# Kernel tuning notes

Hardware: AMD Instinct MI355X
Metric: run time of the kernel (lower is better)

The kernel has to match this reference:

```python
import jax, jax.numpy as jnp
import numpy as np

EPS = 1e-8


def l2norm(x, axis):
    # matches torch: x / (sqrt(sum(x^2)) + eps)
    return x / (jnp.sqrt(jnp.sum(x * x, axis=axis, keepdims=True)) + EPS)


def setup_inputs() -> dict:
    key = jax.random.key(0)
    k1, k2, k3, k4, k5 = jax.random.split(key, 5)
    I, C, L, R, D = 16, 32, 32, 36, 1024  # n_image, n_caption, max_words, n_regions, embed_dim
    img_emb = l2norm(jax.random.normal(k1, (I, R, D), jnp.float32), -1)
    cap_emb = l2norm(jax.random.normal(k2, (C, L, D), jnp.float32), -1)
    W_emb = jax.random.normal(k3, (D, D), jnp.float32)  # nn.Embedding weight, N(0,1) default init
    sim_map_w = 2.5 + 0.1 * jax.random.normal(k4, (1, D), jnp.float32)  # init_weight: normal(2.5, 0.1)
    temp_scale_w = jnp.full((1, 1), np.log(1.0 / 0.07), jnp.float32)    # init_weight
    temp_learnable_w = jnp.full((1, 1), 4.0, jnp.float32)               # init_weight
    cap_lens = jax.random.randint(k5, (C,), 4, L + 1, jnp.int32)        # ragged caption lengths in [4, L]
    return dict(img_emb=img_emb, cap_emb=cap_emb, W_emb=W_emb, sim_map_w=sim_map_w,
                temp_scale_w=temp_scale_w, temp_learnable_w=temp_learnable_w, cap_lens=cap_lens)


def reference(img_emb, cap_emb, W_emb, sim_map_w, temp_scale_w, temp_learnable_w, cap_lens):
    D = W_emb.shape[0]
    L = cap_emb.shape[1]
    # --- dimension-weight branch (caption-independent) ---
    # linspace(0, D, D).long(): last index is D (out of range in torch); gather with clip.
    idx = jnp.floor(jnp.linspace(0.0, D, D)).astype(jnp.int32)
    weights = jax.nn.sigmoid(jnp.take(W_emb, idx, axis=0, mode='clip'))  # (D, D)
    mean_p = jnp.mean(weights, axis=1)                  # (D,)
    std_p = jnp.std(weights, axis=1, ddof=1)            # torch.std is unbiased
    thres = mean_p + sim_map_w[0] * std_p               # (D,)
    values = jnp.exp(temp_learnable_w[0, 0]) * (weights - thres[:, None])
    mask_p = jnp.tanh(jnp.exp(values))
    Dlw = l2norm(mask_p * weights, axis=1)              # Dim_learned_weights (D, D)
    diag = Dlw.sum(0)                                   # Diagonal (D,); diag_embed matmul == elementwise scale
    smooth = jnp.exp(temp_scale_w[0, 0])
    # --- vectorized ragged per-caption cross attention ---
    wmask = (jnp.arange(L)[None, :] < cap_lens[:, None]).astype(cap_emb.dtype)  # (C, L)
    # attn[c,i,l,r] = tanh(sum_d cap[c,l,d] * diag[d] * img[i,r,d])
    attn = jnp.tanh(jnp.einsum('cld,ird->cilr', cap_emb, img_emb * diag))
    attn = jnp.where(attn >= 0, attn, 0.1 * attn) * wmask[:, None, :, None]  # LeakyReLU(0.1), zero padded words
    attn = attn / (jnp.sqrt(jnp.sum(attn * attn, axis=2, keepdims=True)) + EPS)  # l2norm over word dim
    attn = jax.nn.softmax(attn * smooth, axis=3)        # softmax over regions
    ctx = l2norm(jnp.einsum('cilr,ird->cild', attn, img_emb), axis=-1)  # Context_img
    sim_loc = ctx * cap_emb[:, None, :, :]
    sim_sub = jnp.einsum('cild,ed->cile', sim_loc, Dlw)  # sim_loc @ Dlw.T
    sim_vec = l2norm(sim_sub, axis=-1).sum(-1)           # (C, I, L)
    # mean over the n_word valid words of each caption
    sim = jnp.sum(sim_vec * wmask[:, None, :], axis=2) / cap_lens[:, None].astype(cap_emb.dtype)  # (C, I)
    return sim.T  # (n_image, n_caption), matching torch.cat(sim_all, 1)
```

## Files before the change

### kernel.cpp

```cpp
#include <hip/hip_runtime.h>
#include <hip/hip_bf16.h>

#define I_N 16
#define C_N 32
#define L_N 32
#define R_N 36
#define D_N 1024
#define EPSF 1e-8f

typedef _Float16 f16;
typedef __attribute__((ext_vector_type(8))) _Float16 half8;
typedef __attribute__((ext_vector_type(4))) float floatx4;

__device__ __forceinline__ void gl16(const f16* g, f16* l) {
  __builtin_amdgcn_global_load_lds(
      (const __attribute__((address_space(1))) void*)g,
      (__attribute__((address_space(3))) void*)l, 16, 0, 0);
}

__device__ __forceinline__ float fast_tanh(float x) {
  float q = __expf(-2.f * fabsf(x));
  float t = (1.f - q) / (1.f + q);
  return (x >= 0.f) ? t : -t;
}

__device__ __forceinline__ float blk_sum_256(float v, float* red) {
  #pragma unroll
  for (int off = 32; off > 0; off >>= 1) v += __shfl_down(v, off, 64);
  int wid = threadIdx.x >> 6;
  if ((threadIdx.x & 63) == 0) red[wid] = v;
  __syncthreads();
  float s = red[0] + red[1] + red[2] + red[3];
  __syncthreads();
  return s;
}

__global__ __launch_bounds__(256) void k_dlw(const float* __restrict__ W,
    const float* __restrict__ simw, const float* __restrict__ tlw,
    const float* __restrict__ img,
    float* __restrict__ Dlw, f16* __restrict__ DlwH, f16* __restrict__ imgP) {
  int bid = blockIdx.x, tid = threadIdx.x;
  if (bid >= 1024) {
    int row = bid - 1024;
    int i = row / 48, r = row % 48;
    size_t dst = (size_t)row * D_N;
    if (r < R_N) {
      size_t src = ((size_t)i * R_N + r) * D_N;
      #pragma unroll
      for (int k = 0; k < 4; ++k) {
        int j = tid + k * 256;
        imgP[dst + j] = (f16)img[src + j];
      }
    } else {
      #pragma unroll
      for (int k = 0; k < 4; ++k) {
        int j = tid + k * 256;
        imgP[dst + j] = (f16)0.f;
      }
    }
    return;
  }
  int row = bid;
  __shared__ float red[4];
  const float* Wr = W + (size_t)row * D_N;
  float w[4]; float p = 0.f;
  #pragma unroll
  for (int k = 0; k < 4; ++k) {
    int j = tid + k * 256;
    float x = Wr[j];
    w[k] = 1.f / (1.f + __expf(-x));
    p += w[k];
  }
  float S = blk_sum_256(p, red);
  float mean = S * (1.f / 1024.f);
  p = 0.f;
  #pragma unroll
  for (int k = 0; k < 4; ++k) { float d = w[k] - mean; p += d * d; }
  float S2 = blk_sum_256(p, red);
  float stdv = sqrtf(S2 * (1.f / 1023.f));
  float thres = mean + simw[row] * stdv;
  float eT = __expf(tlw[0]);
  float mw[4]; p = 0.f;
  #pragma unroll
  for (int k = 0; k < 4; ++k) {
    float val = eT * (w[k] - thres);
    float y = __expf(val);
    float q = __expf(-2.f * y);
    float mp = (1.f - q) / (1.f + q);
    mw[k] = mp * w[k];
    p += mw[k] * mw[k];
  }
  float S3 = blk_sum_256(p, red);
  float inv = 1.f / (sqrtf(S3) + EPSF);
  #pragma unroll
  for (int k = 0; k < 4; ++k) {
    int j = tid + k * 256;
    float v = mw[k] * inv;
    Dlw[(size_t)row * D_N + j] = v;
    DlwH[(size_t)row * D_N + j] = (f16)v;
  }
}

__global__ __launch_bounds__(256) void k_dpp(const float* __restrict__ Dlw,
    const int* __restrict__ lens, float* __restrict__ dpart,
    int* __restrict__ pfx, int* __restrict__ mp) {
  int bid = blockIdx.x;
  if (bid < 64) {
    int p = bid >> 2;
    int col = (bid & 3) * 256 + threadIdx.x;
    float s = 0.f;
    #pragma unroll 8
    for (int r = p * 64; r < p * 64 + 64; ++r) s += Dlw[(size_t)r * D_N + col];
    dpart[(size_t)p * D_N + col] = s;
  } else if (threadIdx.x < 64) {
    int l = threadIdx.x;
    int v = (l < 32) ? lens[l] : 0;
    int s = v;
    #pragma unroll
    for (int off = 1; off < 32; off <<= 1) {
      int t = __shfl_up(s, off, 64);
      if (l >= off) s += t;
    }
    if (l < 32) pfx[l] = s - v;
    if (l == 31) { pfx[32] = s; mp[0] = s * 16; }
  }
}

__global__ __launch_bounds__(256) void k_capd(const float* __restrict__ dpart,
    const float* __restrict__ cap, f16* __restrict__ capD) {
  __shared__ float dg[D_N];
  int tid = threadIdx.x;
  #pragma unroll
  for (int k = 0; k < 4; ++k) {
    int col = tid + k * 256;
    float s = 0.f;
    #pragma unroll
    for (int p = 0; p < 16; ++p) s += dpart[(size_t)p * D_N + col];
    dg[col] = s;
  }
  __syncthreads();
  size_t base = (size_t)blockIdx.x * D_N;
  #pragma unroll
  for (int k = 0; k < 4; ++k) {
    int j = tid + k * 256;
    capD[base + j] = (f16)(cap[base + j] * dg[j]);
  }
}

__global__ __launch_bounds__(256) void k_qk(const f16* __restrict__ A,
    const f16* __restrict__ B, const int* __restrict__ lens,
    const float* __restrict__ tsw, float* __restrict__ pw) {
  int mt = blockIdx.x;
  int i  = blockIdx.y;
  int tid = threadIdx.x;
  int w = tid >> 6, lane = tid & 63;
  int l15 = lane & 15, h = lane >> 4;
  __shared__ __align__(16) f16 Als[64 * 32];
  __shared__ __align__(16) f16 Bls[48 * 32];
  __shared__ float att[64][49];
  __shared__ float cn[2][R_N];
  floatx4 acc[3];
  #pragma unroll
  for (int nf = 0; nf < 3; ++nf) acc[nf] = (floatx4)0.f;
  int arow = tid >> 2;
  int u = tid & 3;
  int vf = (u | ((arow & 1) << 2)) ^ ((arow >> 1) & 7);
  int wofs = (((arow & 62) | (vf >> 2)) * 32) + (vf & 3) * 8;
  const f16* Ag = A + (size_t)(mt * 64 + arow) * D_N + u * 8;
  const f16* Bg = B + (size_t)(i * 48 + arow) * D_N + u * 8;
  int v2 = (h | ((l15 & 1) << 2)) ^ ((l15 >> 1) & 7);
  int rbit = (v2 >> 2) & 1;
  int pun = (v2 & 3) * 8;
  int aoff = (w * 16 + (l15 & 14) + rbit) * 32 + pun;
  int boff[3];
  #pragma unroll
  for (int nf = 0; nf < 3; ++nf) boff[nf] = (nf * 16 + (l15 & 14) + rbit) * 32 + pun;
  for (int kk = 0; kk < D_N; kk += 32) {
    *(float4*)(&Als[wofs]) = *(const float4*)(Ag + kk);
    if (tid < 192) *(float4*)(&Bls[wofs]) = *(const float4*)(Bg + kk);
    __syncthreads();
    half8 a = *(const half8*)(&Als[aoff]);
    #pragma unroll
    for (int nf = 0; nf < 3; ++nf) {
      half8 b = *(const half8*)(&Bls[boff[nf]]);
      acc[nf] = __builtin_amdgcn_mfma_f32_16x16x32_f16(a, b, acc[nf], 0, 0, 0);
    }
    __syncthreads();
  }
  int len0 = lens[mt * 2], len1 = lens[mt * 2 + 1];
  #pragma unroll
  for (int nf = 0; nf < 3; ++nf)
    #pragma unroll
    for (int j = 0; j < 4; ++j) {
      int ml = w * 16 + h * 4 + j;
      int n = nf * 16 + l15;
      float t = fast_tanh(acc[nf][j]);
      float v = (t >= 0.f) ? t : 0.1f * t;
      int len = (ml >= 32) ? len1 : len0;
      if ((ml & 31) >= len || n >= R_N) v = 0.f;
      att[ml][n] = v;
    }
  __syncthreads();
  for (int e = tid; e < 2 * R_N; e += 256) {
    int cc = e / R_N, r = e % R_N;
    float s = 0.f;
    #pragma unroll
    for (int l = 0; l < 32; ++l) { float a = att[cc * 32 + l][r]; s += a * a; }
    cn[cc][r] = sqrtf(s) + EPSF;
  }
  __syncthreads();
  if (tid < 64) {
    int cc = tid >> 5, l = tid & 31;
    float smooth = __expf(tsw[0]);
    float mx = -3.4e38f;
    #pragma unroll
    for (int r = 0; r < R_N; ++r) {
      float z = att[tid][r] / cn[cc][r] * smooth;
      att[tid][r] = z;
      mx = fmaxf(mx, z);
    }
    float se = 0.f;
    #pragma unroll
    for (int r = 0; r < R_N; ++r) {
      float e2 = __expf(att[tid][r] - mx);
      att[tid][r] = e2;
      se += e2;
    }
    float inv = 1.f / se;
    float* dst = pw + ((size_t)i * 1024 + (mt * 2 + cc) * 32 + l) * R_N;
    #pragma unroll
    for (int r = 0; r < R_N; ++r) dst[r] = att[tid][r] * inv;
  }
}

__global__ __launch_bounds__(256) void k_ctx(const float* __restrict__ pw,
    const f16* __restrict__ imgP, const float* __restrict__ cap,
    const int* __restrict__ lens, const int* __restrict__ pfx,
    f16* __restrict__ slc) {
  int c  = blockIdx.x;
  int i  = blockIdx.y;
  int tid = threadIdx.x;
  int w = tid >> 6;
  int cg = tid & 63;
  int len = lens[c];
  int pf = pfx[c];
  __shared__ float pA[32][R_N];
  __shared__ __align__(16) f16 rows[R_N][1024];
  for (int e = tid; e < 32 * R_N; e += 256) {
    int rr = e / R_N, r = e % R_N;
    pA[rr][r] = pw[((size_t)i * 1024 + c * 32 + rr) * R_N + r];
  }
  const f16* base = imgP + (size_t)i * 48 * D_N;
  #pragma unroll
  for (int t = 0; t < 9; ++t) {
    int rr = w * 9 + t;
    const f16* src = base + (size_t)rr * D_N + cg * 8;
    gl16(src,       &rows[rr][0]);
    gl16(src + 512, &rows[rr][512]);
  }
  __syncthreads();
  int d0 = cg * 8, d1 = 512 + cg * 8;
  #pragma unroll
  for (int sub = 0; sub < 2; ++sub) {
    float acc[4][16];
    #pragma unroll
    for (int j = 0; j < 4; ++j)
      #pragma unroll
      for (int q = 0; q < 16; ++q) acc[j][q] = 0.f;
    for (int k = 0; k < R_N; ++k) {
      half8 h0 = *(const half8*)(&rows[k][d0]);
      half8 h1 = *(const half8*)(&rows[k][d1]);
      float bv[16];
      #pragma unroll
      for (int q = 0; q < 8; ++q) { bv[q] = (float)h0[q]; bv[8 + q] = (float)h1[q]; }
      #pragma unroll
      for (int j = 0; j < 4; ++j) {
        float a = pA[sub * 16 + w * 4 + j][k];
        #pragma unroll
        for (int q = 0; q < 16; ++q) acc[j][q] += a * bv[q];
      }
    }
    #pragma unroll
    for (int j = 0; j < 4; ++j) {
      int l = sub * 16 + w * 4 + j;
      float ss = 0.f;
      #pragma unroll
      for (int q = 0; q < 16; ++q) ss += acc[j][q] * acc[j][q];
      #pragma unroll
      for (int off = 1; off < 64; off <<= 1) ss += __shfl_xor(ss, off, 64);
      if (l < len) {
        float inv = 1.f / (sqrtf(ss) + EPSF);
        const float* capr = cap + ((size_t)c * L_N + l) * D_N;
        float4 c0 = *(const float4*)(capr + d0);
        float4 c1 = *(const float4*)(capr + d0 + 4);
        float4 c2 = *(const float4*)(capr + d1);
        float4 c3 = *(const float4*)(capr + d1 + 4);
        float cv[16] = {c0.x,c0.y,c0.z,c0.w, c1.x,c1.y,c1.z,c1.w,
                        c2.x,c2.y,c2.z,c2.w, c3.x,c3.y,c3.z,c3.w};
        union { f16 h[16]; float4 f4[2]; } u;
        #pragma unroll
        for (int q = 0; q < 16; ++q) u.h[q] = (f16)(acc[j][q] * inv * cv[q]);
        f16* dst = slc + ((size_t)((pf + l) * 16 + i)) * D_N;
        *(float4*)(dst + d0) = u.f4[0];
        *(float4*)(dst + d1) = u.f4[1];
      }
    }
  }
}

__global__ __launch_bounds__(256) void k_gemm(const f16* __restrict__ A,
    const f16* __restrict__ B, const int* __restrict__ mp,
    float* __restrict__ rs16, float* __restrict__ rq16) {
  int bx = blockIdx.x, by = blockIdx.y;
  int Mp = mp[0];
  int m0 = bx * 128, n0 = by * 128;
  if (m0 >= Mp) return;
  int tid = threadIdx.x;
  int w = tid >> 6, lane = tid & 63;
  int l15 = lane & 15, h = lane >> 4;
  int wm = w >> 1, wn = w & 1;
  __shared__ __align__(16) f16 AB[3][2][128 * 32];
  floatx4 acc[4][4];
  #pragma unroll
  for (int mf = 0; mf < 4; ++mf)
    #pragma unroll
    for (int nf = 0; nf < 4; ++nf) acc[mf][nf] = (floatx4)0.f;

  int r_p = lane >> 2, u_p = lane & 3;
  int sw = (r_p >> 1) & 7;
  int val = (u_p | ((r_p & 1) << 2)) ^ sw;
  int r_l = (r_p & 14) | (val >> 2);
  int u_l = val & 3;
  const f16* As0 = A + (size_t)(m0 + w * 32 +  0 + r_l) * D_N + u_l * 8;
  const f16* As1 = A + (size_t)(m0 + w * 32 + 16 + r_l) * D_N + u_l * 8;
  const f16* Bs0 = B + (size_t)(n0 + w * 32 +  0 + r_l) * D_N + u_l * 8;
  const f16* Bs1 = B + (size_t)(n0 + w * 32 + 16 + r_l) * D_N + u_l * 8;

  int v2 = (h | ((l15 & 1) << 2)) ^ ((l15 >> 1) & 7);
  int rbit = (v2 >> 2) & 1;
  int pun = (v2 & 3) * 8;
  int aoff[4], boff[4];
  #pragma unroll
  for (int f = 0; f < 4; ++f) {
    aoff[f] = (wm * 64 + f * 16 + (l15 & 14) + rbit) * 32 + pun;
    boff[f] = (wn * 64 + f * 16 + (l15 & 14) + rbit) * 32 + pun;
  }

  #define STAGE(kt, b) { \
    int kof = (kt) * 32; \
    gl16(As0 + kof, &AB[b][0][(w * 32 +  0) * 32]); \
    gl16(As1 + kof, &AB[b][0][(w * 32 + 16) * 32]); \
    gl16(Bs0 + kof, &AB[b][1][(w * 32 +  0) * 32]); \
    gl16(Bs1 + kof, &AB[b][1][(w * 32 + 16) * 32]); }

  #define COMPUTE(b) { \
    half8 af[4], bf[4]; \
    _Pragma("unroll") for (int f = 0; f < 4; ++f) af[f] = *(const half8*)(&AB[b][0][aoff[f]]); \
    _Pragma("unroll") for (int f = 0; f < 4; ++f) bf[f] = *(const half8*)(&AB[b][1][boff[f]]); \
    _Pragma("unroll") for (int mf = 0; mf < 4; ++mf) \
      _Pragma("unroll") for (int nf = 0; nf < 4; ++nf) \
        acc[mf][nf] = __builtin_amdgcn_mfma_f32_16x16x32_f16(af[mf], bf[nf], acc[mf][nf], 0, 0, 0); }

  STAGE(0, 0);
  STAGE(1, 1);
  int cur = 0, n2 = 2;
  for (int kk = 0; kk < 30; ++kk) {
    STAGE(kk + 2, n2);
    asm volatile("s_waitcnt vmcnt(8)" ::: "memory");
    __builtin_amdgcn_s_barrier();
    __builtin_amdgcn_sched_barrier(0);
    COMPUTE(cur);
    __builtin_amdgcn_s_barrier();
    cur = (cur == 2) ? 0 : cur + 1;
    n2  = (n2  == 2) ? 0 : n2  + 1;
  }
  asm volatile("s_waitcnt vmcnt(4)" ::: "memory");
  __builtin_amdgcn_s_barrier();
  __builtin_amdgcn_sched_barrier(0);
  COMPUTE(cur);
  __builtin_amdgcn_s_barrier();
  cur = (cur == 2) ? 0 : cur + 1;
  asm volatile("s_waitcnt vmcnt(0)" ::: "memory");
  __builtin_amdgcn_s_barrier();
  __builtin_amdgcn_sched_barrier(0);
  COMPUTE(cur);
  #undef STAGE
  #undef COMPUTE

  int slot = by * 2 + wn;
  #pragma unroll
  for (int mf = 0; mf < 4; ++mf)
    #pragma unroll
    for (int j = 0; j < 4; ++j) {
      float s = 0.f, q = 0.f;
      #pragma unroll
      for (int nf = 0; nf < 4; ++nf) { float v = acc[mf][nf][j]; s += v; q += v * v; }
      #pragma unroll
      for (int off = 1; off < 16; off <<= 1) { s += __shfl_xor(s, off, 64); q += __shfl_xor(q, off, 64); }
      if (l15 == 0) {
        int m = m0 + wm * 64 + mf * 16 + h * 4 + j;
        rs16[(size_t)slot * 16384 + m] = s;
        rq16[(size_t)slot * 16384 + m] = q;
      }
    }
}

__global__ __launch_bounds__(64) void k_final(const float* __restrict__ rs16,
    const float* __restrict__ rq16, const int* __restrict__ lens,
    const int* __restrict__ pfx, float* __restrict__ out) {
  int b = blockIdx.x;
  int c = b & 31;
  int l = threadIdx.x;
  int len = lens[c];
  float sv = 0.f;
  if (l < len) {
    int i = b >> 5;
    int row = (pfx[c] + l) * 16 + i;
    float rs = 0.f, rq = 0.f;
    #pragma unroll
    for (int s = 0; s < 16; ++s) {
      rs += rs16[(size_t)s * 16384 + row];
      rq += rq16[(size_t)s * 16384 + row];
    }
    sv = rs / (sqrtf(rq) + EPSF);
  }
  #pragma unroll
  for (int off = 32; off > 0; off >>= 1) sv += __shfl_down(sv, off, 64);
  if (l == 0) out[b] = sv / (float)len;
}

extern "C" void kernel_launch(void* const* d_in, const int* in_sizes, int n_in,
                              void* d_out, int out_size, void* d_ws, size_t ws_size,
                              hipStream_t stream) {
  const float* img  = (const float*)d_in[0];
  const float* cap  = (const float*)d_in[1];
  const float* W    = (const float*)d_in[2];
  const float* simw = (const float*)d_in[3];
  const float* tsw  = (const float*)d_in[4];
  const float* tlw  = (const float*)d_in[5];
  const int*   lens = (const int*)d_in[6];
  float* out = (float*)d_out;

  char* wsB = (char*)d_ws;
  if (ws_size < 51122176) return;
  float* Dlw   = (float*)(wsB + 0);
  f16*   DlwH  = (f16*)  (wsB + 4194304);
  f16*   capD  = (f16*)  (wsB + 6295552);
  f16*   imgP  = (f16*)  (wsB + 8392704);
  float* dpart = (float*)(wsB + 9965568);
  int*   mp    = (int*)  (wsB + 10031104);
  int*   pfx   = (int*)  (wsB + 10031360);
  float* pw    = (float*)(wsB + 13111296);
  f16*   slc   = (f16*)  (wsB + 15470592);
  float* rs16  = (float*)(wsB + 49025024);
  float* rq16  = (float*)(wsB + 50073600);

  k_dlw<<<1792, 256, 0, stream>>>(W, simw, tlw, img, Dlw, DlwH, imgP);
  k_dpp<<<65, 256, 0, stream>>>(Dlw, lens, dpart, pfx, mp);
  k_capd<<<1024, 256, 0, stream>>>(dpart, cap, capD);
  k_qk<<<dim3(16, 16), 256, 0, stream>>>(capD, imgP, lens, tsw, pw);
  k_ctx<<<dim3(32, 16), 256, 0, stream>>>(pw, imgP, cap, lens, pfx, slc);
  k_gemm<<<dim3(128, 8), 256, 0, stream>>>(slc, DlwH, mp, rs16, rq16);
  k_final<<<512, 64, 0, stream>>>(rs16, rq16, lens, pfx, out);
}
```

Baseline: 102.1 us.

## Enlarge GEMM tile to 256x128 with each wave spanning full N width

The sim_sub GEMM tile grows from 128x128 to 256x128. Each wave now owns 64 rows across all 128 columns, so the per-row partial sums of squares cover the whole N tile and the partial slots drop from 16 to 8. This halves the number of blocks and raises the MFMA-to-load ratio for better data reuse. In exchange it uses more accumulator registers and LDS per block, and fewer blocks are launched on a large GPU, which may leave compute units idle.

```diff
diff --git a/kernel.cpp b/kernel.cpp
--- a/kernel.cpp
+++ b/kernel.cpp
@@ -310,63 +310,68 @@
 
 __global__ __launch_bounds__(256) void k_gemm(const f16* __restrict__ A,
     const f16* __restrict__ B, const int* __restrict__ mp,
-    float* __restrict__ rs16, float* __restrict__ rq16) {
+    float* __restrict__ rs8, float* __restrict__ rq8) {
   int bx = blockIdx.x, by = blockIdx.y;
   int Mp = mp[0];
-  int m0 = bx * 128, n0 = by * 128;
+  int m0 = bx * 256, n0 = by * 128;
   if (m0 >= Mp) return;
   int tid = threadIdx.x;
   int w = tid >> 6, lane = tid & 63;
   int l15 = lane & 15, h = lane >> 4;
-  int wm = w >> 1, wn = w & 1;
-  __shared__ __align__(16) f16 AB[3][2][128 * 32];
-  floatx4 acc[4][4];
+  __shared__ __align__(16) f16 As[3][256 * 32];
+  __shared__ __align__(16) f16 Bs[3][128 * 32];
+  floatx4 acc[4][8];
   #pragma unroll
   for (int mf = 0; mf < 4; ++mf)
     #pragma unroll
-    for (int nf = 0; nf < 4; ++nf) acc[mf][nf] = (floatx4)0.f;
+    for (int nf = 0; nf < 8; ++nf) acc[mf][nf] = (floatx4)0.f;
 
   int r_p = lane >> 2, u_p = lane & 3;
   int sw = (r_p >> 1) & 7;
   int val = (u_p | ((r_p & 1) << 2)) ^ sw;
   int r_l = (r_p & 14) | (val >> 2);
   int u_l = val & 3;
-  const f16* As0 = A + (size_t)(m0 + w * 32 +  0 + r_l) * D_N + u_l * 8;
-  const f16* As1 = A + (size_t)(m0 + w * 32 + 16 + r_l) * D_N + u_l * 8;
-  const f16* Bs0 = B + (size_t)(n0 + w * 32 +  0 + r_l) * D_N + u_l * 8;
-  const f16* Bs1 = B + (size_t)(n0 + w * 32 + 16 + r_l) * D_N + u_l * 8;
+  const f16* Ag0 = A + (size_t)(m0 + w * 64 +  0 + r_l) * D_N + u_l * 8;
+  const f16* Ag1 = A + (size_t)(m0 + w * 64 + 16 + r_l) * D_N + u_l * 8;
+  const f16* Ag2 = A + (size_t)(m0 + w * 64 + 32 + r_l) * D_N + u_l * 8;
+  const f16* Ag3 = A + (size_t)(m0 + w * 64 + 48 + r_l) * D_N + u_l * 8;
+  const f16* Bg0 = B + (size_t)(n0 + w * 32 +  0 + r_l) * D_N + u_l * 8;
+  const f16* Bg1 = B + (size_t)(n0 + w * 32 + 16 + r_l) * D_N + u_l * 8;
 
   int v2 = (h | ((l15 & 1) << 2)) ^ ((l15 >> 1) & 7);
   int rbit = (v2 >> 2) & 1;
   int pun = (v2 & 3) * 8;
-  int aoff[4], boff[4];
-  #pragma unroll
-  for (int f = 0; f < 4; ++f) {
-    aoff[f] = (wm * 64 + f * 16 + (l15 & 14) + rbit) * 32 + pun;
-    boff[f] = (wn * 64 + f * 16 + (l15 & 14) + rbit) * 32 + pun;
-  }
+  int aoff[4], boff[8];
+  #pragma unroll
+  for (int f = 0; f < 4; ++f)
+    aoff[f] = (w * 64 + f * 16 + (l15 & 14) + rbit) * 32 + pun;
+  #pragma unroll
+  for (int f = 0; f < 8; ++f)
+    boff[f] = (f * 16 + (l15 & 14) + rbit) * 32 + pun;
 
   #define STAGE(kt, b) { \
     int kof = (kt) * 32; \
-    gl16(As0 + kof, &AB[b][0][(w * 32 +  0) * 32]); \
-    gl16(As1 + kof, &AB[b][0][(w * 32 + 16) * 32]); \
-    gl16(Bs0 + kof, &AB[b][1][(w * 32 +  0) * 32]); \
-    gl16(Bs1 + kof, &AB[b][1][(w * 32 + 16) * 32]); }
+    gl16(Ag0 + kof, &As[b][(w * 64 +  0) * 32]); \
+    gl16(Ag1 + kof, &As[b][(w * 64 + 16) * 32]); \
+    gl16(Ag2 + kof, &As[b][(w * 64 + 32) * 32]); \
+    gl16(Ag3 + kof, &As[b][(w * 64 + 48) * 32]); \
+    gl16(Bg0 + kof, &Bs[b][(w * 32 +  0) * 32]); \
+    gl16(Bg1 + kof, &Bs[b][(w * 32 + 16) * 32]); }
 
   #define COMPUTE(b) { \
-    half8 af[4], bf[4]; \
-    _Pragma("unroll") for (int f = 0; f < 4; ++f) af[f] = *(const half8*)(&AB[b][0][aoff[f]]); \
-    _Pragma("unroll") for (int f = 0; f < 4; ++f) bf[f] = *(const half8*)(&AB[b][1][boff[f]]); \
-    _Pragma("unroll") for (int mf = 0; mf < 4; ++mf) \
-      _Pragma("unroll") for (int nf = 0; nf < 4; ++nf) \
-        acc[mf][nf] = __builtin_amdgcn_mfma_f32_16x16x32_f16(af[mf], bf[nf], acc[mf][nf], 0, 0, 0); }
+    half8 af[4]; \
+    _Pragma("unroll") for (int f = 0; f < 4; ++f) af[f] = *(const half8*)(&As[b][aoff[f]]); \
+    _Pragma("unroll") for (int nf = 0; nf < 8; ++nf) { \
+      half8 bf = *(const half8*)(&Bs[b][boff[nf]]); \
+      _Pragma("unroll") for (int mf = 0; mf < 4; ++mf) \
+        acc[mf][nf] = __builtin_amdgcn_mfma_f32_16x16x32_f16(af[mf], bf, acc[mf][nf], 0, 0, 0); } }
 
   STAGE(0, 0);
   STAGE(1, 1);
   int cur = 0, n2 = 2;
   for (int kk = 0; kk < 30; ++kk) {
     STAGE(kk + 2, n2);
-    asm volatile("s_waitcnt vmcnt(8)" ::: "memory");
+    asm volatile("s_waitcnt vmcnt(12)" ::: "memory");
     __builtin_amdgcn_s_barrier();
     __builtin_amdgcn_sched_barrier(0);
     COMPUTE(cur);
@@ -374,7 +379,7 @@
     cur = (cur == 2) ? 0 : cur + 1;
     n2  = (n2  == 2) ? 0 : n2  + 1;
   }
-  asm volatile("s_waitcnt vmcnt(4)" ::: "memory");
+  asm volatile("s_waitcnt vmcnt(6)" ::: "memory");
   __builtin_amdgcn_s_barrier();
   __builtin_amdgcn_sched_barrier(0);
   COMPUTE(cur);
@@ -387,26 +392,26 @@
   #undef STAGE
   #undef COMPUTE
 
-  int slot = by * 2 + wn;
+  int slot = by;
   #pragma unroll
   for (int mf = 0; mf < 4; ++mf)
     #pragma unroll
     for (int j = 0; j < 4; ++j) {
       float s = 0.f, q = 0.f;
       #pragma unroll
-      for (int nf = 0; nf < 4; ++nf) { float v = acc[mf][nf][j]; s += v; q += v * v; }
+      for (int nf = 0; nf < 8; ++nf) { float v = acc[mf][nf][j]; s += v; q += v * v; }
       #pragma unroll
       for (int off = 1; off < 16; off <<= 1) { s += __shfl_xor(s, off, 64); q += __shfl_xor(q, off, 64); }
       if (l15 == 0) {
-        int m = m0 + wm * 64 + mf * 16 + h * 4 + j;
-        rs16[(size_t)slot * 16384 + m] = s;
-        rq16[(size_t)slot * 16384 + m] = q;
+        int m = m0 + w * 64 + mf * 16 + h * 4 + j;
+        rs8[(size_t)slot * 16384 + m] = s;
+        rq8[(size_t)slot * 16384 + m] = q;
       }
     }
 }
 
-__global__ __launch_bounds__(64) void k_final(const float* __restrict__ rs16,
-    const float* __restrict__ rq16, const int* __restrict__ lens,
+__global__ __launch_bounds__(64) void k_final(const float* __restrict__ rs8,
+    const float* __restrict__ rq8, const int* __restrict__ lens,
     const int* __restrict__ pfx, float* __restrict__ out) {
   int b = blockIdx.x;
   int c = b & 31;
@@ -418,9 +423,9 @@
     int row = (pfx[c] + l) * 16 + i;
     float rs = 0.f, rq = 0.f;
     #pragma unroll
-    for (int s = 0; s < 16; ++s) {
-      rs += rs16[(size_t)s * 16384 + row];
-      rq += rq16[(size_t)s * 16384 + row];
+    for (int s = 0; s < 8; ++s) {
+      rs += rs8[(size_t)s * 16384 + row];
+      rq += rq8[(size_t)s * 16384 + row];
     }
     sv = rs / (sqrtf(rq) + EPSF);
   }
@@ -452,14 +457,14 @@
   int*   pfx   = (int*)  (wsB + 10031360);
   float* pw    = (float*)(wsB + 13111296);
   f16*   slc   = (f16*)  (wsB + 15470592);
-  float* rs16  = (float*)(wsB + 49025024);
-  float* rq16  = (float*)(wsB + 50073600);
+  float* rs8   = (float*)(wsB + 49025024);
+  float* rq8   = (float*)(wsB + 50073600);
 
   k_dlw<<<1792, 256, 0, stream>>>(W, simw, tlw, img, Dlw, DlwH, imgP);
   k_dpp<<<65, 256, 0, stream>>>(Dlw, lens, dpart, pfx, mp);
   k_capd<<<1024, 256, 0, stream>>>(dpart, cap, capD);
   k_qk<<<dim3(16, 16), 256, 0, stream>>>(capD, imgP, lens, tsw, pw);
   k_ctx<<<dim3(32, 16), 256, 0, stream>>>(pw, imgP, cap, lens, pfx, slc);
-  k_gemm<<<dim3(128, 8), 256, 0, stream>>>(slc, DlwH, mp, rs16, rq16);
-  k_final<<<512, 64, 0, stream>>>(rs16, rq16, lens, pfx, out);
-}
+  k_gemm<<<dim3(64, 8), 256, 0, stream>>>(slc, DlwH, mp, rs8, rq8);
+  k_final<<<512, 64, 0, stream>>>(rs8, rq8, lens, pfx, out);
+}
```

Result: slower. 113.5 us (+11.2%).

## Process Dlw rows per wavefront and drop fp32 Dlw buffer

Applied to the files above, without the earlier changes.

The Dlw kernel now gives each 64-lane wavefront one row instead of each 256-thread block. This replaces block-level shared-memory reductions and their barriers with xor-shuffle wave reductions, and uses float4 loads with packed half stores. The fp32 Dlw copy is no longer written, and the column-sum kernel reads the fp16 copy instead, which cuts the writes and reads of a 4 MB buffer. The cost is a slight loss of precision in the diagonal sums, which are now accumulated from fp16 values.

```diff
diff --git a/kernel.cpp b/kernel.cpp
--- a/kernel.cpp
+++ b/kernel.cpp
@@ -24,84 +24,79 @@
   return (x >= 0.f) ? t : -t;
 }
 
-__device__ __forceinline__ float blk_sum_256(float v, float* red) {
-  #pragma unroll
-  for (int off = 32; off > 0; off >>= 1) v += __shfl_down(v, off, 64);
-  int wid = threadIdx.x >> 6;
-  if ((threadIdx.x & 63) == 0) red[wid] = v;
-  __syncthreads();
-  float s = red[0] + red[1] + red[2] + red[3];
-  __syncthreads();
-  return s;
+__device__ __forceinline__ float wave_sum64(float v) {
+  #pragma unroll
+  for (int off = 32; off > 0; off >>= 1) v += __shfl_xor(v, off, 64);
+  return v;
 }
 
 __global__ __launch_bounds__(256) void k_dlw(const float* __restrict__ W,
     const float* __restrict__ simw, const float* __restrict__ tlw,
     const float* __restrict__ img,
-    float* __restrict__ Dlw, f16* __restrict__ DlwH, f16* __restrict__ imgP) {
-  int bid = blockIdx.x, tid = threadIdx.x;
-  if (bid >= 1024) {
-    int row = bid - 1024;
+    f16* __restrict__ DlwH, f16* __restrict__ imgP) {
+  int gw = blockIdx.x * 4 + (threadIdx.x >> 6);
+  int lane = threadIdx.x & 63;
+  if (gw >= 1024) {
+    int row = gw - 1024;
     int i = row / 48, r = row % 48;
     size_t dst = (size_t)row * D_N;
-    if (r < R_N) {
-      size_t src = ((size_t)i * R_N + r) * D_N;
-      #pragma unroll
-      for (int k = 0; k < 4; ++k) {
-        int j = tid + k * 256;
-        imgP[dst + j] = (f16)img[src + j];
+    #pragma unroll
+    for (int q = 0; q < 4; ++q) {
+      int col = lane * 4 + q * 256;
+      f16 h4[4];
+      if (r < R_N) {
+        size_t src = ((size_t)i * R_N + r) * D_N;
+        float4 v = *(const float4*)(img + src + col);
+        h4[0] = (f16)v.x; h4[1] = (f16)v.y; h4[2] = (f16)v.z; h4[3] = (f16)v.w;
+      } else {
+        h4[0] = h4[1] = h4[2] = h4[3] = (f16)0.f;
       }
-    } else {
-      #pragma unroll
-      for (int k = 0; k < 4; ++k) {
-        int j = tid + k * 256;
-        imgP[dst + j] = (f16)0.f;
-      }
+      *(float2*)(imgP + dst + col) = *(float2*)h4;
     }
     return;
   }
-  int row = bid;
-  __shared__ float red[4];
+  int row = gw;
   const float* Wr = W + (size_t)row * D_N;
-  float w[4]; float p = 0.f;
-  #pragma unroll
-  for (int k = 0; k < 4; ++k) {
-    int j = tid + k * 256;
-    float x = Wr[j];
-    w[k] = 1.f / (1.f + __expf(-x));
-    p += w[k];
-  }
-  float S = blk_sum_256(p, red);
+  float w[16]; float p = 0.f;
+  #pragma unroll
+  for (int q = 0; q < 4; ++q) {
+    float4 v = *(const float4*)(Wr + lane * 4 + q * 256);
+    w[q*4+0] = 1.f / (1.f + __expf(-v.x));
+    w[q*4+1] = 1.f / (1.f + __expf(-v.y));
+    w[q*4+2] = 1.f / (1.f + __expf(-v.z));
+    w[q*4+3] = 1.f / (1.f + __expf(-v.w));
+    p += w[q*4+0] + w[q*4+1] + w[q*4+2] + w[q*4+3];
+  }
+  float S = wave_sum64(p);
   float mean = S * (1.f / 1024.f);
   p = 0.f;
   #pragma unroll
-  for (int k = 0; k < 4; ++k) { float d = w[k] - mean; p += d * d; }
-  float S2 = blk_sum_256(p, red);
+  for (int k = 0; k < 16; ++k) { float d = w[k] - mean; p += d * d; }
+  float S2 = wave_sum64(p);
   float stdv = sqrtf(S2 * (1.f / 1023.f));
   float thres = mean + simw[row] * stdv;
   float eT = __expf(tlw[0]);
-  float mw[4]; p = 0.f;
-  #pragma unroll
-  for (int k = 0; k < 4; ++k) {
-    float val = eT * (w[k] - thres);
-    float y = __expf(val);
-    float q = __expf(-2.f * y);
-    float mp = (1.f - q) / (1.f + q);
-    mw[k] = mp * w[k];
-    p += mw[k] * mw[k];
-  }
-  float S3 = blk_sum_256(p, red);
+  p = 0.f;
+  #pragma unroll
+  for (int k = 0; k < 16; ++k) {
+    float y = __expf(eT * (w[k] - thres));
+    float q2 = __expf(-2.f * y);
+    float mp = (1.f - q2) / (1.f + q2);
+    w[k] = mp * w[k];
+    p += w[k] * w[k];
+  }
+  float S3 = wave_sum64(p);
   float inv = 1.f / (sqrtf(S3) + EPSF);
   #pragma unroll
-  for (int k = 0; k < 4; ++k) {
-    int j = tid + k * 256;
-    float v = mw[k] * inv;
-    Dlw[(size_t)row * D_N + j] = v;
-    DlwH[(size_t)row * D_N + j] = (f16)v;
-  }
-}
-
-__global__ __launch_bounds__(256) void k_dpp(const float* __restrict__ Dlw,
+  for (int q = 0; q < 4; ++q) {
+    f16 h4[4];
+    #pragma unroll
+    for (int t = 0; t < 4; ++t) h4[t] = (f16)(w[q*4+t] * inv);
+    *(float2*)(DlwH + (size_t)row * D_N + lane * 4 + q * 256) = *(float2*)h4;
+  }
+}
+
+__global__ __launch_bounds__(256) void k_dpp(const f16* __restrict__ DlwH,
     const int* __restrict__ lens, float* __restrict__ dpart,
     int* __restrict__ pfx, int* __restrict__ mp) {
   int bid = blockIdx.x;
@@ -110,7 +105,7 @@
     int col = (bid & 3) * 256 + threadIdx.x;
     float s = 0.f;
     #pragma unroll 8
-    for (int r = p * 64; r < p * 64 + 64; ++r) s += Dlw[(size_t)r * D_N + col];
+    for (int r = p * 64; r < p * 64 + 64; ++r) s += (float)DlwH[(size_t)r * D_N + col];
     dpart[(size_t)p * D_N + col] = s;
   } else if (threadIdx.x < 64) {
     int l = threadIdx.x;
@@ -443,7 +438,6 @@
 
   char* wsB = (char*)d_ws;
   if (ws_size < 51122176) return;
-  float* Dlw   = (float*)(wsB + 0);
   f16*   DlwH  = (f16*)  (wsB + 4194304);
   f16*   capD  = (f16*)  (wsB + 6295552);
   f16*   imgP  = (f16*)  (wsB + 8392704);
@@ -455,8 +449,8 @@
   float* rs16  = (float*)(wsB + 49025024);
   float* rq16  = (float*)(wsB + 50073600);
 
-  k_dlw<<<1792, 256, 0, stream>>>(W, simw, tlw, img, Dlw, DlwH, imgP);
-  k_dpp<<<65, 256, 0, stream>>>(Dlw, lens, dpart, pfx, mp);
+  k_dlw<<<448, 256, 0, stream>>>(W, simw, tlw, img, DlwH, imgP);
+  k_dpp<<<65, 256, 0, stream>>>(DlwH, lens, dpart, pfx, mp);
   k_capd<<<1024, 256, 0, stream>>>(dpart, cap, capD);
   k_qk<<<dim3(16, 16), 256, 0, stream>>>(capD, imgP, lens, tsw, pw);
   k_ctx<<<dim3(32, 16), 256, 0, stream>>>(pw, imgP, cap, lens, pfx, slc);
```

Result: no change. 101.3 us (-0.8%).
